# Kernel optimization log

Hardware: AMD Instinct MI355X
Metric: run time of the kernel (lower is better)

The kernel has to match this reference:

```python
import jax, jax.numpy as jnp
import numpy as np

B = 2048
D = 256
C = 100000
SCALE = 30.0
MARGIN = 0.2
EPS = 1e-6


def setup_inputs() -> dict:
    key = jax.random.key(0)
    k1, k2, k3 = jax.random.split(key, 3)
    emb = jax.random.normal(k1, (B, D), dtype=jnp.float32)
    # speaker embeddings are typically L2-normalized; also keeps cosines in (-1,1)
    emb = emb / jnp.linalg.norm(emb, axis=1, keepdims=True)
    W = jax.random.normal(k2, (C, D), dtype=jnp.float32)
    targets = jax.random.randint(k3, (B,), 0, C, dtype=jnp.int64)
    return {"embedding": emb, "W": W, "targets": targets}


def reference(embedding, W, targets):
    # normalize classifier rows (F.normalize on weight, dim=1, eps=1e-12)
    Wn = W / jnp.maximum(jnp.linalg.norm(W, axis=1, keepdims=True), 1e-12)
    # [B, C] cosine logits, clamped as in the original
    cos = jnp.clip(embedding @ Wn.T, -1.0, 1.0)
    # per-sample target cosine -> margin-adjusted numerator
    tgt_cos = jnp.take_along_axis(cos, targets[:, None], axis=1)[:, 0]
    numerator = SCALE * jnp.cos(jnp.arccos(tgt_cos) + MARGIN)  # [B]
    # masked sum over non-target classes (replaces the python loop + cat)
    col = jnp.arange(C, dtype=targets.dtype)[None, :]
    not_target = (col != targets[:, None]).astype(cos.dtype)  # [B, C]
    excl_sum = jnp.sum(jnp.exp(SCALE * cos) * not_target, axis=1)  # [B]
    denominator = jnp.exp(numerator) + excl_sum
    loss = -jnp.mean(numerator - jnp.log(denominator + EPS))
    return loss
```

## Files before the change

### kernel.cpp

```cpp
#include <hip/hip_runtime.h>
#include <hip/hip_bf16.h>


static constexpr int Bn = 2048;
static constexpr int Dn = 256;
static constexpr int Cn = 100000;
static constexpr int NSLICE = 1564;
static constexpr int CPAD   = NSLICE * 64;
static constexpr float OOB_COLS = (float)(CPAD - Cn);
static constexpr int NT  = Bn / 16;
static constexpr int NWV = 4;
static constexpr int NTW = NT / NWV;

#define SCALE_F 30.0f
#define MARGIN_F 0.2f
#define EPS_F 1e-6f
#define L2E_SCALE 43.2808512266689f

typedef __attribute__((ext_vector_type(8))) short bf16x8;
typedef __attribute__((ext_vector_type(4))) float f32x4;

__device__ __forceinline__ short f2bf_rne(float x) {
    union { float f; unsigned int u; } v; v.f = x;
    unsigned int r = v.u + 0x7fffu + ((v.u >> 16) & 1u);
    return (short)(r >> 16);
}

__global__ __launch_bounds__(256) void k_prep(const float* __restrict__ W,
                                              const float* __restrict__ emb,
                                              const int* __restrict__ tgt,
                                              short* __restrict__ embF,
                                              float* __restrict__ numv,
                                              float* __restrict__ etv) {
    const int blk = blockIdx.x;
    if (blk < 256) {
        const int t     = blk >> 1;
        const int chunk = (blk & 1) * 256 + threadIdx.x;
        const int ks    = chunk >> 6;
        const int lane  = chunk & 63;
        const int q     = lane >> 4;
        const int cr    = lane & 15;
        const float* src = emb + (size_t)(t * 16 + cr) * Dn + ks * 32 + q * 8;
        float4 x0 = *(const float4*)(src);
        float4 x1 = *(const float4*)(src + 4);
        bf16x8 o;
        o[0] = f2bf_rne(x0.x * L2E_SCALE); o[1] = f2bf_rne(x0.y * L2E_SCALE);
        o[2] = f2bf_rne(x0.z * L2E_SCALE); o[3] = f2bf_rne(x0.w * L2E_SCALE);
        o[4] = f2bf_rne(x1.x * L2E_SCALE); o[5] = f2bf_rne(x1.y * L2E_SCALE);
        o[6] = f2bf_rne(x1.z * L2E_SCALE); o[7] = f2bf_rne(x1.w * L2E_SCALE);
        *(bf16x8*)(embF + (size_t)((t * 8 + ks) * 64 + lane) * 8) = o;
    } else {
        const int b    = (blk - 256) * 4 + (threadIdx.x >> 6);
        const int lane = threadIdx.x & 63;
        const int t    = tgt[b];
        float4 x = *(const float4*)(W + (size_t)t * Dn + lane * 4);
        float4 e = *(const float4*)(emb + b * Dn + lane * 4);
        float dot = x.x * e.x + x.y * e.y + x.z * e.z + x.w * e.w;
        float ss  = x.x * x.x + x.y * x.y + x.z * x.z + x.w * x.w;
#pragma unroll
        for (int o = 1; o < 64; o <<= 1) {
            dot += __shfl_xor(dot, o);
            ss  += __shfl_xor(ss, o);
        }
        if (lane == 0) {
            float cosv = dot / fmaxf(sqrtf(ss), 1e-12f);
            cosv = fminf(fmaxf(cosv, -1.f), 1.f);
            const float num = SCALE_F * cosf(acosf(cosv) + MARGIN_F);
            numv[b] = num;
            etv[b]  = __expf(SCALE_F * cosv);
        }
    }
}

__global__ __launch_bounds__(256, 2) void k_main(const float* __restrict__ W,
                                                 const short* __restrict__ embF,
                                                 float* __restrict__ partial) {
    __shared__ short afrag_sh[4 * 8 * 64 * 8];
    const int tid  = threadIdx.x;
    const int lane = tid & 63;
    const int wv   = tid >> 6;
    const int q    = lane >> 4;
    const int cr   = lane & 15;
    const int sl   = blockIdx.x;
    const int cbase = sl * 64;

    {
        const int c = cbase + wv * 16 + cr;
        const float* wr = W + (size_t)c * Dn;
        float ss = 0.0f;
        if (c < Cn) {
#pragma unroll
            for (int ks = 0; ks < 8; ++ks) {
                float4 x0 = *(const float4*)(wr + ks * 32 + q * 8);
                float4 x1 = *(const float4*)(wr + ks * 32 + q * 8 + 4);
                ss += x0.x * x0.x + x0.y * x0.y + x0.z * x0.z + x0.w * x0.w;
                ss += x1.x * x1.x + x1.y * x1.y + x1.z * x1.z + x1.w * x1.w;
            }
        }
        ss += __shfl_xor(ss, 16);
        ss += __shfl_xor(ss, 32);
        const float rn = 1.0f / fmaxf(sqrtf(ss), 1e-12f);
#pragma unroll
        for (int ks = 0; ks < 8; ++ks) {
            bf16x8 a = {0, 0, 0, 0, 0, 0, 0, 0};
            if (c < Cn) {
                float4 x0 = *(const float4*)(wr + ks * 32 + q * 8);
                float4 x1 = *(const float4*)(wr + ks * 32 + q * 8 + 4);
                a[0] = f2bf_rne(x0.x * rn); a[1] = f2bf_rne(x0.y * rn);
                a[2] = f2bf_rne(x0.z * rn); a[3] = f2bf_rne(x0.w * rn);
                a[4] = f2bf_rne(x1.x * rn); a[5] = f2bf_rne(x1.y * rn);
                a[6] = f2bf_rne(x1.z * rn); a[7] = f2bf_rne(x1.w * rn);
            }
            *(bf16x8*)(afrag_sh + (size_t)((wv * 8 + ks) * 64 + lane) * 8) = a;
        }
    }
    __syncthreads();

    bf16x8 afrag[4][8];
#pragma unroll
    for (int ct = 0; ct < 4; ++ct)
#pragma unroll
        for (int ks = 0; ks < 8; ++ks)
            afrag[ct][ks] = *(const bf16x8*)(afrag_sh + (size_t)((ct * 8 + ks) * 64 + lane) * 8);

    float* pout = partial + (size_t)sl * Bn;
    const bf16x8* bsrc = (const bf16x8*)embF;
    const int t0 = wv * NTW;

    auto load_b = [&](bf16x8* bf, int t) {
        const bf16x8* p = bsrc + (size_t)t * 512 + lane;
#pragma unroll
        for (int ks = 0; ks < 8; ++ks) bf[ks] = p[ks * 64];
    };

    auto compute = [&](const bf16x8* bf, int t) {
        f32x4 a0 = {0.f, 0.f, 0.f, 0.f};
        f32x4 a1 = {0.f, 0.f, 0.f, 0.f};
        f32x4 a2 = {0.f, 0.f, 0.f, 0.f};
        f32x4 a3 = {0.f, 0.f, 0.f, 0.f};
#pragma unroll
        for (int ks = 0; ks < 8; ++ks) {
            a0 = __builtin_amdgcn_mfma_f32_16x16x32_bf16(afrag[0][ks], bf[ks], a0, 0, 0, 0);
            a1 = __builtin_amdgcn_mfma_f32_16x16x32_bf16(afrag[1][ks], bf[ks], a1, 0, 0, 0);
            a2 = __builtin_amdgcn_mfma_f32_16x16x32_bf16(afrag[2][ks], bf[ks], a2, 0, 0, 0);
            a3 = __builtin_amdgcn_mfma_f32_16x16x32_bf16(afrag[3][ks], bf[ks], a3, 0, 0, 0);
        }
        float s0 = 0.f, s1 = 0.f, s2 = 0.f, s3 = 0.f;
#pragma unroll
        for (int r = 0; r < 4; ++r) {
            s0 += __builtin_amdgcn_exp2f(a0[r]);
            s1 += __builtin_amdgcn_exp2f(a1[r]);
            s2 += __builtin_amdgcn_exp2f(a2[r]);
            s3 += __builtin_amdgcn_exp2f(a3[r]);
        }
        float s = (s0 + s1) + (s2 + s3);
        s += __shfl_xor(s, 16);
        s += __shfl_xor(s, 32);
        if (lane < 16) pout[t * 16 + cr] = s;
    };

    bf16x8 b0[8], b1[8];
    load_b(b0, t0);
    for (int i = 0; i < NTW; i += 2) {
        load_b(b1, t0 + i + 1);
        compute(b0, t0 + i);
        load_b(b0, (i + 2) < NTW ? (t0 + i + 2) : t0);
        compute(b1, t0 + i + 1);
    }
}

__global__ __launch_bounds__(256) void k_finish(const float* __restrict__ partial,
                                                const float* __restrict__ numv,
                                                const float* __restrict__ etv,
                                                float* __restrict__ out) {
    __shared__ float red[64];
    const int l  = threadIdx.x & 63;
    const int qq = threadIdx.x >> 6;
    const int b  = blockIdx.x * 64 + l;

    if (threadIdx.x < 64) red[threadIdx.x] = 0.0f;
    __syncthreads();

    const int s0 = qq * (NSLICE / 4);
    const int s1 = s0 + (NSLICE / 4);
    float acc = 0.0f;
    for (int s = s0; s < s1; ++s) acc += partial[(size_t)s * Bn + b];
    atomicAdd(&red[l], acc);
    __syncthreads();

    if (threadIdx.x < 64) {
        const float num  = numv[b];
        const float excl = red[l] - OOB_COLS - etv[b];
        const float denom = __expf(num) + excl;
        float term = num - logf(denom + EPS_F);
#pragma unroll
        for (int o = 1; o < 64; o <<= 1) term += __shfl_xor(term, o);
        if (l == 0) atomicAdd(out, -term / (float)Bn);
    }
}

extern "C" void kernel_launch(void* const* d_in, const int* in_sizes, int n_in,
                              void* d_out, int out_size, void* d_ws, size_t ws_size,
                              hipStream_t stream) {
    const float* emb = (const float*)d_in[0];
    const float* W   = (const float*)d_in[1];
    const int*   tgt = (const int*)d_in[2];
    float* out = (float*)d_out;

    char* ws = (char*)d_ws;
    short* embF    = (short*)ws;
    float* partial = (float*)(ws + (1 << 20));
    float* numv    = partial + (size_t)NSLICE * Bn;
    float* etv     = numv + Bn;

    hipMemsetAsync(out, 0, sizeof(float), stream);
    k_prep<<<768, 256, 0, stream>>>(W, emb, tgt, embF, numv, etv);
    k_main<<<NSLICE, 256, 0, stream>>>(W, embF, partial);
    k_finish<<<32, 256, 0, stream>>>(partial, numv, etv, out);
}
```

Before: 258.8 us.

## Read W fragments from LDS per MFMA and double waves per block

The main kernel now runs 8 waves per 512-thread block instead of 4. Each wave handles half as many batch tiles, and the normalized W fragments stay in shared memory and are read on every k-step, no longer held in 32 register vectors. W row normalization is restructured so each row is read once, with eight lanes per row, and the embedding prefetch is issued before that prologue. Partial sums are written at half-reduced granularity (32 per tile), so the finish kernel is rewritten to sum both halves across twice the data. The aim is lower register pressure and higher occupancy, at the cost of extra LDS traffic in the inner loop and a larger partial buffer to reduce.

```diff
diff --git a/kernel.cpp b/kernel.cpp
--- a/kernel.cpp
+++ b/kernel.cpp
@@ -9,7 +9,7 @@
 static constexpr int CPAD   = NSLICE * 64;
 static constexpr float OOB_COLS = (float)(CPAD - Cn);
 static constexpr int NT  = Bn / 16;
-static constexpr int NWV = 4;
+static constexpr int NWV = 8;
 static constexpr int NTW = NT / NWV;
 
 #define SCALE_F 30.0f
@@ -72,58 +72,16 @@
     }
 }
 
-__global__ __launch_bounds__(256, 2) void k_main(const float* __restrict__ W,
+__global__ __launch_bounds__(512, 4) void k_main(const float* __restrict__ W,
                                                  const short* __restrict__ embF,
                                                  float* __restrict__ partial) {
     __shared__ short afrag_sh[4 * 8 * 64 * 8];
     const int tid  = threadIdx.x;
     const int lane = tid & 63;
     const int wv   = tid >> 6;
-    const int q    = lane >> 4;
-    const int cr   = lane & 15;
     const int sl   = blockIdx.x;
     const int cbase = sl * 64;
 
-    {
-        const int c = cbase + wv * 16 + cr;
-        const float* wr = W + (size_t)c * Dn;
-        float ss = 0.0f;
-        if (c < Cn) {
-#pragma unroll
-            for (int ks = 0; ks < 8; ++ks) {
-                float4 x0 = *(const float4*)(wr + ks * 32 + q * 8);
-                float4 x1 = *(const float4*)(wr + ks * 32 + q * 8 + 4);
-                ss += x0.x * x0.x + x0.y * x0.y + x0.z * x0.z + x0.w * x0.w;
-                ss += x1.x * x1.x + x1.y * x1.y + x1.z * x1.z + x1.w * x1.w;
-            }
-        }
-        ss += __shfl_xor(ss, 16);
-        ss += __shfl_xor(ss, 32);
-        const float rn = 1.0f / fmaxf(sqrtf(ss), 1e-12f);
-#pragma unroll
-        for (int ks = 0; ks < 8; ++ks) {
-            bf16x8 a = {0, 0, 0, 0, 0, 0, 0, 0};
-            if (c < Cn) {
-                float4 x0 = *(const float4*)(wr + ks * 32 + q * 8);
-                float4 x1 = *(const float4*)(wr + ks * 32 + q * 8 + 4);
-                a[0] = f2bf_rne(x0.x * rn); a[1] = f2bf_rne(x0.y * rn);
-                a[2] = f2bf_rne(x0.z * rn); a[3] = f2bf_rne(x0.w * rn);
-                a[4] = f2bf_rne(x1.x * rn); a[5] = f2bf_rne(x1.y * rn);
-                a[6] = f2bf_rne(x1.z * rn); a[7] = f2bf_rne(x1.w * rn);
-            }
-            *(bf16x8*)(afrag_sh + (size_t)((wv * 8 + ks) * 64 + lane) * 8) = a;
-        }
-    }
-    __syncthreads();
-
-    bf16x8 afrag[4][8];
-#pragma unroll
-    for (int ct = 0; ct < 4; ++ct)
-#pragma unroll
-        for (int ks = 0; ks < 8; ++ks)
-            afrag[ct][ks] = *(const bf16x8*)(afrag_sh + (size_t)((ct * 8 + ks) * 64 + lane) * 8);
-
-    float* pout = partial + (size_t)sl * Bn;
     const bf16x8* bsrc = (const bf16x8*)embF;
     const int t0 = wv * NTW;
 
@@ -132,6 +90,47 @@
 #pragma unroll
         for (int ks = 0; ks < 8; ++ks) bf[ks] = p[ks * 64];
     };
+
+    bf16x8 b0[8], b1[8];
+    load_b(b0, t0);
+
+    {
+        const int ks  = lane & 7;
+        const int rlo = wv * 8 + (lane >> 3);
+        const int c   = cbase + rlo;
+        const int ct  = rlo >> 4;
+        const int crr = rlo & 15;
+        float v[32];
+        if (c < Cn) {
+            const float* wr = W + (size_t)c * Dn + ks * 32;
+#pragma unroll
+            for (int j = 0; j < 8; ++j) {
+                float4 x = *(const float4*)(wr + j * 4);
+                v[j * 4 + 0] = x.x; v[j * 4 + 1] = x.y;
+                v[j * 4 + 2] = x.z; v[j * 4 + 3] = x.w;
+            }
+        } else {
+#pragma unroll
+            for (int j = 0; j < 32; ++j) v[j] = 0.0f;
+        }
+        float ss = 0.0f;
+#pragma unroll
+        for (int j = 0; j < 32; ++j) ss += v[j] * v[j];
+        ss += __shfl_xor(ss, 1);
+        ss += __shfl_xor(ss, 2);
+        ss += __shfl_xor(ss, 4);
+        const float rn = 1.0f / fmaxf(sqrtf(ss), 1e-12f);
+#pragma unroll
+        for (int q2 = 0; q2 < 4; ++q2) {
+            bf16x8 a;
+#pragma unroll
+            for (int j = 0; j < 8; ++j) a[j] = f2bf_rne(v[q2 * 8 + j] * rn);
+            *(bf16x8*)(afrag_sh + (size_t)(((ct * 8 + ks) * 64) + q2 * 16 + crr) * 8) = a;
+        }
+    }
+    __syncthreads();
+
+    float* pout = partial + (size_t)sl * (NT * 32);
 
     auto compute = [&](const bf16x8* bf, int t) {
         f32x4 a0 = {0.f, 0.f, 0.f, 0.f};
@@ -140,10 +139,15 @@
         f32x4 a3 = {0.f, 0.f, 0.f, 0.f};
 #pragma unroll
         for (int ks = 0; ks < 8; ++ks) {
-            a0 = __builtin_amdgcn_mfma_f32_16x16x32_bf16(afrag[0][ks], bf[ks], a0, 0, 0, 0);
-            a1 = __builtin_amdgcn_mfma_f32_16x16x32_bf16(afrag[1][ks], bf[ks], a1, 0, 0, 0);
-            a2 = __builtin_amdgcn_mfma_f32_16x16x32_bf16(afrag[2][ks], bf[ks], a2, 0, 0, 0);
-            a3 = __builtin_amdgcn_mfma_f32_16x16x32_bf16(afrag[3][ks], bf[ks], a3, 0, 0, 0);
+            const short* ap = afrag_sh + (size_t)(ks * 64 + lane) * 8;
+            bf16x8 w0 = *(const bf16x8*)(ap);
+            bf16x8 w1 = *(const bf16x8*)(ap + 4096);
+            bf16x8 w2 = *(const bf16x8*)(ap + 8192);
+            bf16x8 w3 = *(const bf16x8*)(ap + 12288);
+            a0 = __builtin_amdgcn_mfma_f32_16x16x32_bf16(w0, bf[ks], a0, 0, 0, 0);
+            a1 = __builtin_amdgcn_mfma_f32_16x16x32_bf16(w1, bf[ks], a1, 0, 0, 0);
+            a2 = __builtin_amdgcn_mfma_f32_16x16x32_bf16(w2, bf[ks], a2, 0, 0, 0);
+            a3 = __builtin_amdgcn_mfma_f32_16x16x32_bf16(w3, bf[ks], a3, 0, 0, 0);
         }
         float s0 = 0.f, s1 = 0.f, s2 = 0.f, s3 = 0.f;
 #pragma unroll
@@ -154,13 +158,10 @@
             s3 += __builtin_amdgcn_exp2f(a3[r]);
         }
         float s = (s0 + s1) + (s2 + s3);
-        s += __shfl_xor(s, 16);
         s += __shfl_xor(s, 32);
-        if (lane < 16) pout[t * 16 + cr] = s;
+        if (lane < 32) pout[t * 32 + lane] = s;
     };
 
-    bf16x8 b0[8], b1[8];
-    load_b(b0, t0);
     for (int i = 0; i < NTW; i += 2) {
         load_b(b1, t0 + i + 1);
         compute(b0, t0 + i);
@@ -173,29 +174,34 @@
                                                 const float* __restrict__ numv,
                                                 const float* __restrict__ etv,
                                                 float* __restrict__ out) {
-    __shared__ float red[64];
-    const int l  = threadIdx.x & 63;
-    const int qq = threadIdx.x >> 6;
-    const int b  = blockIdx.x * 64 + l;
-
-    if (threadIdx.x < 64) red[threadIdx.x] = 0.0f;
+    __shared__ float red[32];
+    const int l     = threadIdx.x & 31;
+    const int chunk = threadIdx.x >> 5;
+    const int b  = blockIdx.x * 32 + l;
+    const int t  = b >> 4;
+    const int cr = b & 15;
+
+    if (threadIdx.x < 32) red[threadIdx.x] = 0.0f;
     __syncthreads();
 
-    const int s0 = qq * (NSLICE / 4);
-    const int s1 = s0 + (NSLICE / 4);
     float acc = 0.0f;
-    for (int s = s0; s < s1; ++s) acc += partial[(size_t)s * Bn + b];
-    atomicAdd(&red[l], acc);
+    const int i0 = chunk * 391, i1 = i0 + 391;
+    for (int idx = i0; idx < i1; ++idx) {
+        const int s = idx >> 1, h = idx & 1;
+        acc += partial[(size_t)s * (NT * 32) + t * 32 + h * 16 + cr];
+    }
+    acc += __shfl_xor(acc, 32);
+    if ((threadIdx.x & 63) < 32) atomicAdd(&red[l], acc);
     __syncthreads();
 
-    if (threadIdx.x < 64) {
-        const float num  = numv[b];
-        const float excl = red[l] - OOB_COLS - etv[b];
-        const float denom = __expf(num) + excl;
-        float term = num - logf(denom + EPS_F);
-#pragma unroll
-        for (int o = 1; o < 64; o <<= 1) term += __shfl_xor(term, o);
-        if (l == 0) atomicAdd(out, -term / (float)Bn);
+    if (threadIdx.x < 32) {
+        const int bb = blockIdx.x * 32 + threadIdx.x;
+        const float num  = numv[bb];
+        const float excl = red[threadIdx.x] - OOB_COLS - etv[bb];
+        float term = num - logf(__expf(num) + excl + EPS_F);
+#pragma unroll
+        for (int o = 1; o < 32; o <<= 1) term += __shfl_xor(term, o);
+        if (threadIdx.x == 0) atomicAdd(out, -term / (float)Bn);
     }
 }
 
@@ -210,11 +216,11 @@
     char* ws = (char*)d_ws;
     short* embF    = (short*)ws;
     float* partial = (float*)(ws + (1 << 20));
-    float* numv    = partial + (size_t)NSLICE * Bn;
+    float* numv    = partial + (size_t)NSLICE * (NT * 32);
     float* etv     = numv + Bn;
 
     hipMemsetAsync(out, 0, sizeof(float), stream);
     k_prep<<<768, 256, 0, stream>>>(W, emb, tgt, embF, numv, etv);
-    k_main<<<NSLICE, 256, 0, stream>>>(W, embF, partial);
-    k_finish<<<32, 256, 0, stream>>>(partial, numv, etv, out);
-}
+    k_main<<<NSLICE, 512, 0, stream>>>(W, embF, partial);
+    k_finish<<<64, 256, 0, stream>>>(partial, numv, etv, out);
+}
```

New measurement: 720.2 us. 178% more time.

## Process 32-row batch tiles per MFMA step, read W fragments from LDS, widen finish

Applied to the files above, without the earlier changes.

The main kernel now handles two 16-row embedding tiles per step, so each W fragment read from shared memory feeds two MFMAs. W fragments are no longer held in registers across the loop but re-read from LDS each k-step, which frees registers to hold a doubled B buffer; launch bounds drop to one block per SIMD-pair hint. The finish kernel spreads the slice reduction over 128 blocks with 16 samples each and uses shuffles before the shared atomic, giving it more parallelism. In exchange the main loop takes more LDS traffic and may run at lower occupancy.

```diff
diff --git a/kernel.cpp b/kernel.cpp
--- a/kernel.cpp
+++ b/kernel.cpp
@@ -8,7 +8,7 @@
 static constexpr int NSLICE = 1564;
 static constexpr int CPAD   = NSLICE * 64;
 static constexpr float OOB_COLS = (float)(CPAD - Cn);
-static constexpr int NT  = Bn / 16;
+static constexpr int NT  = Bn / 32;
 static constexpr int NWV = 4;
 static constexpr int NTW = NT / NWV;
 
@@ -72,7 +72,7 @@
     }
 }
 
-__global__ __launch_bounds__(256, 2) void k_main(const float* __restrict__ W,
+__global__ __launch_bounds__(256, 1) void k_main(const float* __restrict__ W,
                                                  const short* __restrict__ embF,
                                                  float* __restrict__ partial) {
     __shared__ short afrag_sh[4 * 8 * 64 * 8];
@@ -116,50 +116,60 @@
     }
     __syncthreads();
 
-    bf16x8 afrag[4][8];
-#pragma unroll
-    for (int ct = 0; ct < 4; ++ct)
-#pragma unroll
-        for (int ks = 0; ks < 8; ++ks)
-            afrag[ct][ks] = *(const bf16x8*)(afrag_sh + (size_t)((ct * 8 + ks) * 64 + lane) * 8);
-
     float* pout = partial + (size_t)sl * Bn;
     const bf16x8* bsrc = (const bf16x8*)embF;
     const int t0 = wv * NTW;
 
-    auto load_b = [&](bf16x8* bf, int t) {
-        const bf16x8* p = bsrc + (size_t)t * 512 + lane;
-#pragma unroll
-        for (int ks = 0; ks < 8; ++ks) bf[ks] = p[ks * 64];
+    auto load_b = [&](bf16x8 (&bf)[2][8], int t) {
+        const bf16x8* p = bsrc + ((size_t)(2 * t) * 512) + lane;
+#pragma unroll
+        for (int h = 0; h < 2; ++h)
+#pragma unroll
+            for (int ks = 0; ks < 8; ++ks) bf[h][ks] = p[h * 512 + ks * 64];
     };
 
-    auto compute = [&](const bf16x8* bf, int t) {
-        f32x4 a0 = {0.f, 0.f, 0.f, 0.f};
-        f32x4 a1 = {0.f, 0.f, 0.f, 0.f};
-        f32x4 a2 = {0.f, 0.f, 0.f, 0.f};
-        f32x4 a3 = {0.f, 0.f, 0.f, 0.f};
+    auto compute = [&](bf16x8 (&bf)[2][8], int t) {
+        f32x4 acc[4][2];
+#pragma unroll
+        for (int ct = 0; ct < 4; ++ct)
+#pragma unroll
+            for (int h = 0; h < 2; ++h) acc[ct][h] = (f32x4){0.f, 0.f, 0.f, 0.f};
 #pragma unroll
         for (int ks = 0; ks < 8; ++ks) {
-            a0 = __builtin_amdgcn_mfma_f32_16x16x32_bf16(afrag[0][ks], bf[ks], a0, 0, 0, 0);
-            a1 = __builtin_amdgcn_mfma_f32_16x16x32_bf16(afrag[1][ks], bf[ks], a1, 0, 0, 0);
-            a2 = __builtin_amdgcn_mfma_f32_16x16x32_bf16(afrag[2][ks], bf[ks], a2, 0, 0, 0);
-            a3 = __builtin_amdgcn_mfma_f32_16x16x32_bf16(afrag[3][ks], bf[ks], a3, 0, 0, 0);
-        }
-        float s0 = 0.f, s1 = 0.f, s2 = 0.f, s3 = 0.f;
-#pragma unroll
-        for (int r = 0; r < 4; ++r) {
-            s0 += __builtin_amdgcn_exp2f(a0[r]);
-            s1 += __builtin_amdgcn_exp2f(a1[r]);
-            s2 += __builtin_amdgcn_exp2f(a2[r]);
-            s3 += __builtin_amdgcn_exp2f(a3[r]);
-        }
-        float s = (s0 + s1) + (s2 + s3);
-        s += __shfl_xor(s, 16);
-        s += __shfl_xor(s, 32);
-        if (lane < 16) pout[t * 16 + cr] = s;
+            const short* ap = afrag_sh + (size_t)(ks * 64 + lane) * 8;
+            bf16x8 w0 = *(const bf16x8*)(ap);
+            bf16x8 w1 = *(const bf16x8*)(ap + 4096);
+            bf16x8 w2 = *(const bf16x8*)(ap + 8192);
+            bf16x8 w3 = *(const bf16x8*)(ap + 12288);
+            acc[0][0] = __builtin_amdgcn_mfma_f32_16x16x32_bf16(w0, bf[0][ks], acc[0][0], 0, 0, 0);
+            acc[0][1] = __builtin_amdgcn_mfma_f32_16x16x32_bf16(w0, bf[1][ks], acc[0][1], 0, 0, 0);
+            acc[1][0] = __builtin_amdgcn_mfma_f32_16x16x32_bf16(w1, bf[0][ks], acc[1][0], 0, 0, 0);
+            acc[1][1] = __builtin_amdgcn_mfma_f32_16x16x32_bf16(w1, bf[1][ks], acc[1][1], 0, 0, 0);
+            acc[2][0] = __builtin_amdgcn_mfma_f32_16x16x32_bf16(w2, bf[0][ks], acc[2][0], 0, 0, 0);
+            acc[2][1] = __builtin_amdgcn_mfma_f32_16x16x32_bf16(w2, bf[1][ks], acc[2][1], 0, 0, 0);
+            acc[3][0] = __builtin_amdgcn_mfma_f32_16x16x32_bf16(w3, bf[0][ks], acc[3][0], 0, 0, 0);
+            acc[3][1] = __builtin_amdgcn_mfma_f32_16x16x32_bf16(w3, bf[1][ks], acc[3][1], 0, 0, 0);
+        }
+        float sh[2];
+#pragma unroll
+        for (int h = 0; h < 2; ++h) {
+            float s0 = 0.f, s1 = 0.f, s2 = 0.f, s3 = 0.f;
+#pragma unroll
+            for (int ct = 0; ct < 4; ++ct) {
+                s0 += __builtin_amdgcn_exp2f(acc[ct][h][0]);
+                s1 += __builtin_amdgcn_exp2f(acc[ct][h][1]);
+                s2 += __builtin_amdgcn_exp2f(acc[ct][h][2]);
+                s3 += __builtin_amdgcn_exp2f(acc[ct][h][3]);
+            }
+            float s = (s0 + s1) + (s2 + s3);
+            s += __shfl_xor(s, 16);
+            s += __shfl_xor(s, 32);
+            sh[h] = s;
+        }
+        if (lane < 32) pout[t * 32 + lane] = (lane < 16) ? sh[0] : sh[1];
     };
 
-    bf16x8 b0[8], b1[8];
+    bf16x8 b0[2][8], b1[2][8];
     load_b(b0, t0);
     for (int i = 0; i < NTW; i += 2) {
         load_b(b1, t0 + i + 1);
@@ -173,29 +183,29 @@
                                                 const float* __restrict__ numv,
                                                 const float* __restrict__ etv,
                                                 float* __restrict__ out) {
-    __shared__ float red[64];
-    const int l  = threadIdx.x & 63;
-    const int qq = threadIdx.x >> 6;
-    const int b  = blockIdx.x * 64 + l;
-
-    if (threadIdx.x < 64) red[threadIdx.x] = 0.0f;
+    __shared__ float red[16];
+    const int l     = threadIdx.x & 15;
+    const int chunk = threadIdx.x >> 4;
+    const int b  = blockIdx.x * 16 + l;
+
+    if (threadIdx.x < 16) red[threadIdx.x] = 0.0f;
     __syncthreads();
 
-    const int s0 = qq * (NSLICE / 4);
-    const int s1 = s0 + (NSLICE / 4);
     float acc = 0.0f;
-    for (int s = s0; s < s1; ++s) acc += partial[(size_t)s * Bn + b];
-    atomicAdd(&red[l], acc);
+    for (int s = chunk; s < NSLICE; s += 16) acc += partial[(size_t)s * Bn + b];
+    acc += __shfl_xor(acc, 16);
+    acc += __shfl_xor(acc, 32);
+    if ((threadIdx.x & 63) < 16) atomicAdd(&red[l], acc);
     __syncthreads();
 
-    if (threadIdx.x < 64) {
-        const float num  = numv[b];
-        const float excl = red[l] - OOB_COLS - etv[b];
-        const float denom = __expf(num) + excl;
-        float term = num - logf(denom + EPS_F);
-#pragma unroll
-        for (int o = 1; o < 64; o <<= 1) term += __shfl_xor(term, o);
-        if (l == 0) atomicAdd(out, -term / (float)Bn);
+    if (threadIdx.x < 16) {
+        const int bb = blockIdx.x * 16 + threadIdx.x;
+        const float num  = numv[bb];
+        const float excl = red[threadIdx.x] - OOB_COLS - etv[bb];
+        float term = num - logf(__expf(num) + excl + EPS_F);
+#pragma unroll
+        for (int o = 1; o < 16; o <<= 1) term += __shfl_xor(term, o);
+        if (threadIdx.x == 0) atomicAdd(out, -term / (float)Bn);
     }
 }
 
@@ -216,5 +226,5 @@
     hipMemsetAsync(out, 0, sizeof(float), stream);
     k_prep<<<768, 256, 0, stream>>>(W, emb, tgt, embF, numv, etv);
     k_main<<<NSLICE, 256, 0, stream>>>(W, embF, partial);
-    k_finish<<<32, 256, 0, stream>>>(partial, numv, etv, out);
-}
+    k_finish<<<128, 256, 0, stream>>>(partial, numv, etv, out);
+}
```

Measured after the change: 299.0 us. +15.5%, slower.
